# Kernel tuning notes

Hardware: AMD Instinct MI355X
Metric: run time of the kernel (lower is better)

## Reference

```python
import jax, jax.numpy as jnp
import numpy as np

N_QUBITS = 16
N_LAYERS = 4
BATCH = 512


def _apply_1q(state, U, q):
    # state: (B,) + (2,)*n complex64; U: (B,2,2) complex64; acts on qubit q
    s = jnp.moveaxis(state, 1 + q, 1)
    s = jnp.einsum('bij,bj...->bi...', U, s)
    return jnp.moveaxis(s, 1, 1 + q)


def _ry(a):
    # batched RY(a): (B,2,2)
    c = jnp.cos(a / 2)
    s = jnp.sin(a / 2)
    U = jnp.stack([jnp.stack([c, -s], -1), jnp.stack([s, c], -1)], -2)
    return U.astype(jnp.complex64)


def _rot(phi, theta, omega):
    # PennyLane Rot(phi,theta,omega) = RZ(omega) @ RY(theta) @ RZ(phi)
    c = jnp.cos(theta / 2)
    s = jnp.sin(theta / 2)
    U = jnp.stack([
        jnp.stack([jnp.exp(-0.5j * (phi + omega)) * c, -jnp.exp(0.5j * (phi - omega)) * s]),
        jnp.stack([jnp.exp(-0.5j * (phi - omega)) * s, jnp.exp(0.5j * (phi + omega)) * c]),
    ])
    return U.astype(jnp.complex64)


def _cnot(state, ctrl, tgt):
    # flip target axis where control == 1
    s = jnp.moveaxis(state, (1 + ctrl, 1 + tgt), (1, 2))
    s = jnp.concatenate([s[:, 0:1], s[:, 1:2, ::-1]], axis=1)
    return jnp.moveaxis(s, (1, 2), (1 + ctrl, 1 + tgt))


def setup_inputs() -> dict:
    key = jax.random.key(0)
    k1, k2 = jax.random.split(key)
    inputs = jax.random.normal(k1, (BATCH, N_QUBITS), dtype=jnp.float32)
    params = jax.random.normal(k2, (N_LAYERS, N_QUBITS, 3), dtype=jnp.float32)
    return {"inputs": inputs, "params": params}


def reference(inputs, params):
    B = inputs.shape[0]
    n = N_QUBITS
    # |0...0> statevector, one per batch element
    state = jnp.zeros((B, 2 ** n), jnp.complex64).at[:, 0].set(1.0)
    state = state.reshape((B,) + (2,) * n)
    # RY feature map (angle differs per batch element)
    for i in range(n):
        state = _apply_1q(state, _ry(inputs[:, i]), i)
    # variational layers: Rot on each wire, then CNOT chain
    for layer in range(N_LAYERS):
        for i in range(n):
            U = _rot(params[layer, i, 0], params[layer, i, 1], params[layer, i, 2])
            state = _apply_1q(state, jnp.broadcast_to(U, (B, 2, 2)), i)
        for i in range(n - 1):
            state = _cnot(state, i, i + 1)
    # <Z> on wire 0
    probs = jnp.abs(state.reshape(B, 2, -1)) ** 2
    return (probs[:, 0].sum(-1) - probs[:, 1].sum(-1)).astype(jnp.float32)
```

## Files before the change

kernel.cpp:

```cpp
#include <hip/hip_runtime.h>


#define NQ 16

__device__ __forceinline__ float2 cmul(float2 a, float2 b){
    return make_float2(a.x*b.x - a.y*b.y, a.x*b.y + a.y*b.x);
}
__device__ __forceinline__ float2 cmulc(float2 a, float2 b){
    return make_float2(a.x*b.x + a.y*b.y, a.x*b.y - a.y*b.x);
}
__device__ __forceinline__ void cfma(float2& acc, float2 a, float2 b){
    acc.x = fmaf(a.x, b.x, fmaf(-a.y, b.y, acc.x));
    acc.y = fmaf(a.x, b.y, fmaf( a.y, b.x, acc.y));
}
__device__ __forceinline__ void cfmac(float2& acc, float2 a, float2 b){
    acc.x = fmaf(a.x, b.x, fmaf( a.y, b.y, acc.x));
    acc.y = fmaf(a.x, b.y, fmaf(-a.y, b.x, acc.y));
}

__device__ __forceinline__ void make_rot(const float* __restrict__ params, int L, int q, float u[8]){
    const float* pp = params + (L*NQ + q)*3;
    float phi = pp[0], th = pp[1], om = pp[2];
    float s, c;     sincosf(0.5f*th, &s, &c);
    float sap, cap; sincosf(0.5f*(phi+om), &sap, &cap);
    float sam, cam; sincosf(0.5f*(phi-om), &sam, &cam);
    u[0] =  c*cap; u[1] = -c*sap;
    u[2] = -s*cam; u[3] = -s*sam;
    u[4] =  s*cam; u[5] = -s*sam;
    u[6] =  c*cap; u[7] =  c*sap;
}
__device__ __forceinline__ void fuse_ry(float a, float u[8]){
    float sa, ca; sincosf(0.5f*a, &sa, &ca);
    float f0r =  u[0]*ca + u[2]*sa, f0i =  u[1]*ca + u[3]*sa;
    float f1r = -u[0]*sa + u[2]*ca, f1i = -u[1]*sa + u[3]*ca;
    float g0r =  u[4]*ca + u[6]*sa, g0i =  u[5]*ca + u[7]*sa;
    float g1r = -u[4]*sa + u[6]*ca, g1i = -u[5]*sa + u[7]*ca;
    u[0]=f0r; u[1]=f0i; u[2]=f1r; u[3]=f1i; u[4]=g0r; u[5]=g0i; u[6]=g1r; u[7]=g1i;
}

__launch_bounds__(64)
__global__ void qmps_kernel(const float* __restrict__ inputs,
                            const float* __restrict__ params,
                            float* __restrict__ out)
{
    __shared__ __align__(16) float2 U[3][NQ][2][2];
    __shared__ __align__(16) float2 v[NQ][2];
    __shared__ __align__(16) float2 w[14][2][8][10];
    __shared__ __align__(16) float2 Lam[2][2][2][8][10];
    __shared__ __align__(16) float2 Tt[2][2][8][18];
    __shared__ __align__(16) float2 B0[2][8];
    __shared__ __align__(16) float2 r15s[8][2];

    const int t = threadIdx.x;
    const int b = blockIdx.x;

    if (t < 48) {
        int l = t >> 4, q = t & 15;
        float u[8]; make_rot(params, l+1, q, u);
        U[l][q][0][0] = make_float2(u[0],u[1]); U[l][q][0][1] = make_float2(u[2],u[3]);
        U[l][q][1][0] = make_float2(u[4],u[5]); U[l][q][1][1] = make_float2(u[6],u[7]);
    } else {
        int q = t - 48;
        float u[8]; make_rot(params, 0, q, u);
        fuse_ry(inputs[b*NQ + q], u);
        v[q][0] = make_float2(u[0],u[1]);
        v[q][1] = make_float2(u[4],u[5]);
    }
    __syncthreads();

    #pragma unroll 4
    for (int kk = 0; kk < 28; ++kk) {
        int e     = t + (kk << 6);
        int ws    = e >> 7;
        int idx   = e & 127;
        int alpha = idx & 7, beta = (idx >> 3) & 7, m = (idx >> 6) & 1;
        int site  = ws + 1;
        int uu = (site <= 7) ? alpha : beta;
        int dd = (site <= 7) ? beta  : alpha;
        int c1 = uu & 1, c2 = (uu >> 1) & 1, c3 = (uu >> 2) & 1;
        int d1 = dd & 1, d2 = (dd >> 1) & 1, d3 = (dd >> 2) & 1;
        float2 val = cmul(U[2][site][m][d3],
                     cmul(U[1][site][d3^c3][d2],
                     cmul(U[0][site][d2^c2][d1], v[site][d1^c1])));
        w[ws][m][beta][alpha] = val;
    }
    if (t < 16) {
        int j = t >> 3, ap = t & 7;
        int d1 = ap & 1, d2 = (ap>>1)&1, d3 = (ap>>2)&1;
        B0[j][ap] = cmul(U[2][0][j][d3],
                    cmul(U[1][0][d3][d2],
                    cmul(U[0][0][d2][d1], v[0][d1])));
    } else if (t < 32) {
        int t2 = t - 16;
        int a = t2 >> 1, k = t2 & 1;
        int c1 = a & 1, c2 = (a>>1)&1, c3 = (a>>2)&1;
        float2 in1[2], in2[2];
        #pragma unroll
        for (int s2 = 0; s2 < 2; ++s2) {
            float2 acc = make_float2(0.f, 0.f);
            #pragma unroll
            for (int s1 = 0; s1 < 2; ++s1) cfma(acc, U[0][15][s2^c2][s1], v[15][s1^c1]);
            in1[s2] = acc;
        }
        #pragma unroll
        for (int s3 = 0; s3 < 2; ++s3) {
            float2 acc = make_float2(0.f, 0.f);
            #pragma unroll
            for (int s2 = 0; s2 < 2; ++s2) cfma(acc, U[1][15][s3^c3][s2], in1[s2]);
            in2[s3] = acc;
        }
        float2 acc = make_float2(0.f, 0.f);
        #pragma unroll
        for (int s3 = 0; s3 < 2; ++s3) cfma(acc, U[2][15][k][s3], in2[s3]);
        r15s[a][k] = acc;
    }
    __syncthreads();

    #pragma unroll
    for (int h = 0; h < 2; ++h) {
        int e = t + (h << 6);
        int c = e >> 6, aa = (e >> 3) & 7, ap = e & 7;
        float2 valL = cmulc(B0[c][aa], B0[c][ap]);
        float  s    = c ? -1.f : 1.f;
        Lam[0][0][c][aa][ap] = make_float2(s*valL.x, s*valL.y);
        float2 valR = cmulc(r15s[aa][0], r15s[ap][0]);
        cfmac(valR, r15s[aa][1], r15s[ap][1]);
        Lam[1][0][c][aa][ap] = valR;
    }
    __syncthreads();

    int cur = 0;
    #pragma unroll
    for (int k = 0; k < 7; ++k) {
        {
            const int c = t >> 5, a = (t >> 2) & 7, bq = t & 3;
            const int r = c*8 + a;
            #pragma unroll
            for (int env = 0; env < 2; ++env) {
                const int slot = env ? (13 - k) : k;
                const float2* X = &Lam[env][cur][c][a][0];
                float2 xr[8];
                #pragma unroll
                for (int ap = 0; ap < 8; ++ap) xr[ap] = X[ap];
                #pragma unroll
                for (int j = 0; j < 2; ++j) {
                    const float2* w0 = &w[slot][j^c][bq  ][0];
                    const float2* w1 = &w[slot][j^c][bq+4][0];
                    float2 acc0 = make_float2(0.f,0.f), acc1 = make_float2(0.f,0.f);
                    #pragma unroll
                    for (int ap = 0; ap < 8; ++ap) {
                        cfma(acc0, xr[ap], w0[ap]);
                        cfma(acc1, xr[ap], w1[ap]);
                    }
                    Tt[env][j][bq  ][r] = acc0;
                    Tt[env][j][bq+4][r] = acc1;
                }
            }
        }
        __syncthreads();
        {
            const int j = t >> 5, bb = (t >> 2) & 7, bq = t & 3;
            #pragma unroll
            for (int env = 0; env < 2; ++env) {
                const int slot = env ? (13 - k) : k;
                const float2* p0 = &w[slot][j  ][bb][0];
                const float2* p1 = &w[slot][j^1][bb][0];
                float2 wr0[8], wr1[8];
                #pragma unroll
                for (int a2 = 0; a2 < 8; ++a2) { wr0[a2] = p0[a2]; wr1[a2] = p1[a2]; }
                #pragma unroll
                for (int h = 0; h < 2; ++h) {
                    const int bp = bq + (h << 2);
                    const float2* trow = &Tt[env][j][bp][0];
                    float2 acc = make_float2(0.f, 0.f);
                    #pragma unroll
                    for (int a2 = 0; a2 < 8; ++a2) cfmac(acc, wr0[a2], trow[a2]);
                    #pragma unroll
                    for (int a2 = 0; a2 < 8; ++a2) cfmac(acc, wr1[a2], trow[8 + a2]);
                    Lam[env][cur^1][j][bb][bp] = acc;
                }
            }
        }
        __syncthreads();
        cur ^= 1;
    }

    float m = 0.f;
    #pragma unroll
    for (int h = 0; h < 2; ++h) {
        int e = t + (h << 6);
        int c = e >> 6, aa = (e >> 3) & 7, ap = e & 7;
        float2 L = Lam[0][cur][c][aa][ap];
        float2 R = Lam[1][cur][c][aa][ap];
        m += L.x*R.x - L.y*R.y;
    }
    #pragma unroll
    for (int off = 32; off > 0; off >>= 1) m += __shfl_down(m, off, 64);
    if (t == 0) out[b] = m;
}

extern "C" void kernel_launch(void* const* d_in, const int* in_sizes, int n_in,
                              void* d_out, int out_size, void* d_ws, size_t ws_size,
                              hipStream_t stream) {
    (void)n_in; (void)out_size; (void)d_ws; (void)ws_size;
    const float* inputs = (const float*)d_in[0];
    const float* params = (const float*)d_in[1];
    float* out = (float*)d_out;
    const int B = in_sizes[0] / NQ;
    qmps_kernel<<<B, 64, 0, stream>>>(inputs, params, out);
}
```

Before: 69.16 us.

## Keep environment matrices in registers and contract via cross-lane permutes

```diff
diff --git a/kernel.cpp b/kernel.cpp
--- a/kernel.cpp
+++ b/kernel.cpp
@@ -16,6 +16,11 @@
 __device__ __forceinline__ void cfmac(float2& acc, float2 a, float2 b){
     acc.x = fmaf(a.x, b.x, fmaf( a.y, b.y, acc.x));
     acc.y = fmaf(a.x, b.y, fmaf(-a.y, b.x, acc.y));
+}
+__device__ __forceinline__ float2 shfl2(float2 v, int bidx){
+    int x = __builtin_amdgcn_ds_bpermute(bidx, __float_as_int(v.x));
+    int y = __builtin_amdgcn_ds_bpermute(bidx, __float_as_int(v.y));
+    return make_float2(__int_as_float(x), __int_as_float(y));
 }
 
 __device__ __forceinline__ void make_rot(const float* __restrict__ params, int L, int q, float u[8]){
@@ -38,6 +43,16 @@
     u[0]=f0r; u[1]=f0i; u[2]=f1r; u[3]=f1i; u[4]=g0r; u[5]=g0i; u[6]=g1r; u[7]=g1i;
 }
 
+__device__ __forceinline__ void load_col(const float2* __restrict__ p, float2 dst[8]){
+    const float4* q = (const float4*)p;
+    #pragma unroll
+    for (int h = 0; h < 4; ++h) {
+        float4 f = q[h];
+        dst[2*h]   = make_float2(f.x, f.y);
+        dst[2*h+1] = make_float2(f.z, f.w);
+    }
+}
+
 __launch_bounds__(64)
 __global__ void qmps_kernel(const float* __restrict__ inputs,
                             const float* __restrict__ params,
@@ -45,10 +60,8 @@
 {
     __shared__ __align__(16) float2 U[3][NQ][2][2];
     __shared__ __align__(16) float2 v[NQ][2];
-    __shared__ __align__(16) float2 w[14][2][8][10];
-    __shared__ __align__(16) float2 Lam[2][2][2][8][10];
-    __shared__ __align__(16) float2 Tt[2][2][8][18];
-    __shared__ __align__(16) float2 B0[2][8];
+    __shared__ __align__(16) float2 wc[14][2][8][10];
+    __shared__ __align__(16) float2 B0s[2][8];
     __shared__ __align__(16) float2 r15s[8][2];
 
     const int t = threadIdx.x;
@@ -82,14 +95,14 @@
         float2 val = cmul(U[2][site][m][d3],
                      cmul(U[1][site][d3^c3][d2],
                      cmul(U[0][site][d2^c2][d1], v[site][d1^c1])));
-        w[ws][m][beta][alpha] = val;
+        wc[ws][m][beta][alpha] = val;
     }
     if (t < 16) {
-        int j = t >> 3, ap = t & 7;
+        int jj = t >> 3, ap = t & 7;
         int d1 = ap & 1, d2 = (ap>>1)&1, d3 = (ap>>2)&1;
-        B0[j][ap] = cmul(U[2][0][j][d3],
-                    cmul(U[1][0][d3][d2],
-                    cmul(U[0][0][d2][d1], v[0][d1])));
+        B0s[jj][ap] = cmul(U[2][0][jj][d3],
+                      cmul(U[1][0][d3][d2],
+                      cmul(U[0][0][d2][d1], v[0][d1])));
     } else if (t < 32) {
         int t2 = t - 16;
         int a = t2 >> 1, k = t2 & 1;
@@ -116,84 +129,70 @@
     }
     __syncthreads();
 
-    #pragma unroll
-    for (int h = 0; h < 2; ++h) {
-        int e = t + (h << 6);
-        int c = e >> 6, aa = (e >> 3) & 7, ap = e & 7;
-        float2 valL = cmulc(B0[c][aa], B0[c][ap]);
-        float  s    = c ? -1.f : 1.f;
-        Lam[0][0][c][aa][ap] = make_float2(s*valL.x, s*valL.y);
-        float2 valR = cmulc(r15s[aa][0], r15s[ap][0]);
-        cfmac(valR, r15s[aa][1], r15s[ap][1]);
-        Lam[1][0][c][aa][ap] = valR;
-    }
-    __syncthreads();
-
-    int cur = 0;
-    #pragma unroll
-    for (int k = 0; k < 7; ++k) {
-        {
-            const int c = t >> 5, a = (t >> 2) & 7, bq = t & 3;
-            const int r = c*8 + a;
-            #pragma unroll
-            for (int env = 0; env < 2; ++env) {
-                const int slot = env ? (13 - k) : k;
-                const float2* X = &Lam[env][cur][c][a][0];
-                float2 xr[8];
-                #pragma unroll
-                for (int ap = 0; ap < 8; ++ap) xr[ap] = X[ap];
-                #pragma unroll
-                for (int j = 0; j < 2; ++j) {
-                    const float2* w0 = &w[slot][j^c][bq  ][0];
-                    const float2* w1 = &w[slot][j^c][bq+4][0];
-                    float2 acc0 = make_float2(0.f,0.f), acc1 = make_float2(0.f,0.f);
-                    #pragma unroll
-                    for (int ap = 0; ap < 8; ++ap) {
-                        cfma(acc0, xr[ap], w0[ap]);
-                        cfma(acc1, xr[ap], w1[ap]);
-                    }
-                    Tt[env][j][bq  ][r] = acc0;
-                    Tt[env][j][bq+4][r] = acc1;
-                }
-            }
-        }
-        __syncthreads();
-        {
-            const int j = t >> 5, bb = (t >> 2) & 7, bq = t & 3;
-            #pragma unroll
-            for (int env = 0; env < 2; ++env) {
-                const int slot = env ? (13 - k) : k;
-                const float2* p0 = &w[slot][j  ][bb][0];
-                const float2* p1 = &w[slot][j^1][bb][0];
-                float2 wr0[8], wr1[8];
-                #pragma unroll
-                for (int a2 = 0; a2 < 8; ++a2) { wr0[a2] = p0[a2]; wr1[a2] = p1[a2]; }
-                #pragma unroll
-                for (int h = 0; h < 2; ++h) {
-                    const int bp = bq + (h << 2);
-                    const float2* trow = &Tt[env][j][bp][0];
-                    float2 acc = make_float2(0.f, 0.f);
-                    #pragma unroll
-                    for (int a2 = 0; a2 < 8; ++a2) cfmac(acc, wr0[a2], trow[a2]);
-                    #pragma unroll
-                    for (int a2 = 0; a2 < 8; ++a2) cfmac(acc, wr1[a2], trow[8 + a2]);
-                    Lam[env][cur^1][j][bb][bp] = acc;
-                }
-            }
-        }
-        __syncthreads();
-        cur ^= 1;
-    }
-
-    float m = 0.f;
-    #pragma unroll
-    for (int h = 0; h < 2; ++h) {
-        int e = t + (h << 6);
-        int c = e >> 6, aa = (e >> 3) & 7, ap = e & 7;
-        float2 L = Lam[0][cur][c][aa][ap];
-        float2 R = Lam[1][cur][c][aa][ap];
-        m += L.x*R.x - L.y*R.y;
-    }
+    const int i = t >> 3, j = t & 7;
+    float2 LamL0, LamL1, LamR0, LamR1;
+    {
+        LamL0 = cmulc(B0s[0][i], B0s[0][j]);
+        float2 l1 = cmulc(B0s[1][i], B0s[1][j]);
+        LamL1 = make_float2(-l1.x, -l1.y);
+        float2 r = cmulc(r15s[i][0], r15s[j][0]);
+        cfmac(r, r15s[i][1], r15s[j][1]);
+        LamR0 = r; LamR1 = r;
+    }
+
+    const int iA0 = (t << 2) & 0xE0;
+    const int jB0 = (t & 7) << 2;
+
+    #pragma unroll 1
+    for (int st = 0; st < 7; ++st) {
+        const int sL = st, sR = 13 - st;
+        float2 W1L[2][8], W2L[2][8], W1R[2][8], W2R[2][8];
+        #pragma unroll
+        for (int m = 0; m < 2; ++m) {
+            load_col(&wc[sL][m][j][0], W1L[m]);
+            load_col(&wc[sL][m][i][0], W2L[m]);
+            load_col(&wc[sR][m][j][0], W1R[m]);
+            load_col(&wc[sR][m][i][0], W2R[m]);
+        }
+        float2 PL00 = make_float2(0.f,0.f), PL01 = make_float2(0.f,0.f);
+        float2 PL10 = make_float2(0.f,0.f), PL11 = make_float2(0.f,0.f);
+        float2 PR00 = make_float2(0.f,0.f), PR01 = make_float2(0.f,0.f);
+        float2 PR10 = make_float2(0.f,0.f), PR11 = make_float2(0.f,0.f);
+        #pragma unroll
+        for (int k = 0; k < 8; ++k) {
+            const int iA = iA0 | (k << 2);
+            float2 a0 = shfl2(LamL0, iA);
+            float2 a1 = shfl2(LamL1, iA);
+            float2 b0 = shfl2(LamR0, iA);
+            float2 b1 = shfl2(LamR1, iA);
+            cfma(PL00, a0, W1L[0][k]); cfma(PL01, a0, W1L[1][k]);
+            cfma(PL10, a1, W1L[0][k]); cfma(PL11, a1, W1L[1][k]);
+            cfma(PR00, b0, W1R[0][k]); cfma(PR01, b0, W1R[1][k]);
+            cfma(PR10, b1, W1R[0][k]); cfma(PR11, b1, W1R[1][k]);
+        }
+        float2 nL0 = make_float2(0.f,0.f), nL1 = make_float2(0.f,0.f);
+        float2 nR0 = make_float2(0.f,0.f), nR1 = make_float2(0.f,0.f);
+        #pragma unroll
+        for (int k = 0; k < 8; ++k) {
+            const int iB = jB0 | (k << 5);
+            float2 p00 = shfl2(PL00, iB);
+            float2 p01 = shfl2(PL01, iB);
+            float2 p10 = shfl2(PL10, iB);
+            float2 p11 = shfl2(PL11, iB);
+            cfmac(nL0, W2L[0][k], p00); cfmac(nL0, W2L[1][k], p11);
+            cfmac(nL1, W2L[1][k], p01); cfmac(nL1, W2L[0][k], p10);
+            float2 q00 = shfl2(PR00, iB);
+            float2 q01 = shfl2(PR01, iB);
+            float2 q10 = shfl2(PR10, iB);
+            float2 q11 = shfl2(PR11, iB);
+            cfmac(nR0, W2R[0][k], q00); cfmac(nR0, W2R[1][k], q11);
+            cfmac(nR1, W2R[1][k], q01); cfmac(nR1, W2R[0][k], q10);
+        }
+        LamL0 = nL0; LamL1 = nL1; LamR0 = nR0; LamR1 = nR1;
+    }
+
+    float m = LamL0.x*LamR0.x - LamL0.y*LamR0.y
+            + LamL1.x*LamR1.x - LamL1.y*LamR1.y;
     #pragma unroll
     for (int off = 32; off > 0; off >>= 1) m += __shfl_down(m, off, 64);
     if (t == 0) out[b] = m;
```

Result: slower. 72.35 us (+4.6%).
